# Kernel optimization log

Hardware: AMD Instinct MI355X
Metric: run time of the kernel (lower is better)

The kernel has to match this reference:

```python
import jax, jax.numpy as jnp
import numpy as np

N = 8192
INPUT_DIM = 256
HIDDEN_DIM = 16
K_NEIGHBORS = 6


def setup_inputs() -> dict:
    key = jax.random.key(0)
    k1, k2 = jax.random.split(key)
    x = jax.random.normal(k1, (N, INPUT_DIM), dtype=jnp.float32)
    W = jax.random.normal(k2, (HIDDEN_DIM, INPUT_DIM), dtype=jnp.float32) * (1.0 / np.sqrt(INPUT_DIM))
    b = jnp.zeros((HIDDEN_DIM,), dtype=jnp.float32)
    return {"x": x, "W": W, "b": b}


def reference(x, W, b):
    num_nodes = x.shape[0]
    # Linear projection then L2-normalize rows (F.normalize, p=2, dim=1, eps=1e-12)
    h = x @ W.T + b                                   # [N, H]
    norm = jnp.linalg.norm(h, axis=1, keepdims=True)
    h = h / jnp.maximum(norm, 1e-12)
    sim = h @ h.T                                     # [N, N] cosine similarity
    k = min(K_NEIGHBORS, num_nodes - 1)
    # top-(k+1) per row; drop the first (self, sim=1 is the max)
    top_vals, top_idx = jax.lax.top_k(sim, k + 1)     # [N, k+1]
    neigh_idx = top_idx[:, 1:]                        # [N, k]
    neigh_vals = top_vals[:, 1:]                      # [N, k]
    rows = jnp.arange(num_nodes)[:, None]             # [N, 1]
    adj = jnp.zeros_like(sim).at[rows, neigh_idx].set(neigh_vals)
    adj = (adj + adj.T) * 0.5
    row_sums = adj.sum(axis=1, keepdims=True)
    adj = adj / (row_sums + 1e-8)
    return adj
```

## Files before the change

kernel.cpp:

```cpp
#include <hip/hip_runtime.h>
#include <stdint.h>
#include <math.h>

#define NN   8192
#define IND  256
#define HID  16
#define KN   6
#define SEG  8
#define SW   (NN/SEG)
#define CCOL 256
#define NCH  (SW/CCOL)
#define TPC  (CCOL/16)
#define ZPB  8192

typedef short s8v  __attribute__((ext_vector_type(8)));
typedef float f4v  __attribute__((ext_vector_type(4)));

__device__ __forceinline__ uint32_t fflip(float f) {
    const uint32_t u = __float_as_uint(f);
    return (u & 0x80000000u) ? ~u : (u | 0x80000000u);
}

__device__ __forceinline__ uint32_t bf16_rne_bits(float x) {
    const uint32_t u = __float_as_uint(x);
    return (u + 0x7FFFu + ((u >> 16) & 1u)) & 0xFFFF0000u;
}

__global__ __launch_bounds__(256) void k1_embed(const float* __restrict__ x,
                                                const float* __restrict__ W,
                                                const float* __restrict__ b,
                                                float* __restrict__ h,
                                                float* __restrict__ rs)
{
    const int lane = threadIdx.x & 63;
    const int wv   = threadIdx.x >> 6;
    const int row  = blockIdx.x * 4 + wv;

    const float4 xv = *(const float4*)(x + (size_t)row * IND + lane * 4);

    float acc[HID];
#pragma unroll
    for (int k = 0; k < HID; ++k) {
        const float4 wv4 = *(const float4*)(W + (size_t)k * IND + lane * 4);
        float v = xv.x * wv4.x + xv.y * wv4.y + xv.z * wv4.z + xv.w * wv4.w;
#pragma unroll
        for (int m = 32; m >= 1; m >>= 1) v += __shfl_xor(v, m, 64);
        acc[k] = v;
    }

    if (lane == 0) {
        float hv[HID];
        float ss = 0.f;
#pragma unroll
        for (int k = 0; k < HID; ++k) { hv[k] = acc[k] + b[k]; ss += hv[k] * hv[k]; }
        const float nrm = fmaxf(sqrtf(ss), 1e-12f);
#pragma unroll
        for (int k = 0; k < HID; ++k) hv[k] = hv[k] / nrm;
        float4* hp = (float4*)(h + (size_t)row * HID);
        hp[0] = make_float4(hv[0],  hv[1],  hv[2],  hv[3]);
        hp[1] = make_float4(hv[4],  hv[5],  hv[6],  hv[7]);
        hp[2] = make_float4(hv[8],  hv[9],  hv[10], hv[11]);
        hp[3] = make_float4(hv[12], hv[13], hv[14], hv[15]);
        rs[row] = 0.f;
    }
}

__global__ __launch_bounds__(256) void k1b_split(const float* __restrict__ h,
                                                 ushort* __restrict__ PA1,
                                                 ushort* __restrict__ PA2,
                                                 ushort* __restrict__ PA3,
                                                 ushort* __restrict__ PB1,
                                                 ushort* __restrict__ PB2)
{
    const int t   = blockIdx.x * 256 + threadIdx.x;
    const int row = t >> 5;
    const int s   = t & 31;
    const int k   = s & 15;

    const float x = h[(size_t)row * HID + k];
    const uint32_t hb = bf16_rne_bits(x);
    const float r1 = x - __uint_as_float(hb);
    const uint32_t mb = bf16_rne_bits(r1);
    const float r2 = r1 - __uint_as_float(mb);
    const uint32_t lb = bf16_rne_bits(r2);
    const ushort hi = (ushort)(hb >> 16);
    const ushort mi = (ushort)(mb >> 16);
    const ushort lo = (ushort)(lb >> 16);

    const bool f = (s < 16);
    PA1[t] = hi;
    PA2[t] = f ? mi : hi;
    PA3[t] = f ? lo : mi;
    PB1[t] = f ? hi : mi;
    PB2[t] = f ? hi : lo;
}

#define CSWPF(X,i,j) { const float _h = fmaxf(X[i], X[j]); const float _l = fminf(X[i], X[j]); X[i] = _h; X[j] = _l; }
#define CSWPV(a,b)   { const float _h = fmaxf(a, b); const float _l = fminf(a, b); a = _h; b = _l; }
#define BSTAGES(X) CSWPF(X,0,4) CSWPF(X,1,5) CSWPF(X,2,6) CSWPF(X,3,7) \
                   CSWPF(X,0,2) CSWPF(X,1,3) CSWPF(X,4,6) CSWPF(X,5,7) \
                   CSWPF(X,0,1) CSWPF(X,2,3) CSWPF(X,4,5) CSWPF(X,6,7)

__global__ __launch_bounds__(256, 4) void p1_scan(const ushort* __restrict__ PA1,
                                                  const ushort* __restrict__ PA2,
                                                  const ushort* __restrict__ PA3,
                                                  const ushort* __restrict__ PB1,
                                                  const ushort* __restrict__ PB2,
                                                  float* __restrict__ tq,
                                                  float4* __restrict__ outz)
{
    __shared__ s8v lds[2048];

    const int tid  = threadIdx.x;
    const int lane = tid & 63;
    const int wv   = tid >> 6;
    const int seg  = blockIdx.x & (SEG - 1);
    const int row0 = (blockIdx.x >> 3) * 64 + wv * 16;
    const int n    = lane & 15;
    const int q    = lane >> 4;
    const int qs   = (q + ((n >> 1) & 3)) & 3;

    const size_t ioff = ((size_t)(row0 + n) << 5) + (q << 3);
    const s8v i1 = *(const s8v*)(PA1 + ioff);
    const s8v i2 = *(const s8v*)(PA2 + ioff);
    const s8v i3 = *(const s8v*)(PA3 + ioff);

    const float4 zf = make_float4(0.f, 0.f, 0.f, 0.f);

    float L[8];
#pragma unroll
    for (int t = 0; t < 8; ++t) L[t] = -INFINITY;

    for (int cc = 0; cc < NCH; ++cc) {
        __syncthreads();
#pragma unroll
        for (int it = 0; it < 8; ++it) {
            const int o  = it * 256 + tid;
            const int oo = o & 1023;
            const int c  = oo >> 2;
            const int qq = oo & 3;
            const int sw = (qq + ((c >> 1) & 3)) & 3;
            const ushort* src = (it < 4) ? PB1 : PB2;
            const int gcol = seg * SW + cc * CCOL + c;
            const s8v v = *(const s8v*)(src + ((size_t)gcol << 5) + (qq << 3));
            lds[((it < 4) ? 0 : 1024) + (c << 2) + sw] = v;
        }
        __syncthreads();

        {
            const size_t zb = (size_t)blockIdx.x * ZPB + (size_t)cc * 2048 + tid;
#pragma unroll
            for (int z = 0; z < 8; ++z)
                outz[zb + z * 256] = zf;
        }

        const int base = (n << 2) + qs;
#pragma unroll 4
        for (int t = 0; t < TPC; ++t) {
            const s8v jb1 = lds[t * 64 + base];
            const s8v jb2 = lds[1024 + t * 64 + base];

            f4v acc = {0.f, 0.f, 0.f, 0.f};
            acc = __builtin_amdgcn_mfma_f32_16x16x32_bf16(jb1, i1, acc, 0, 0, 0);
            acc = __builtin_amdgcn_mfma_f32_16x16x32_bf16(jb2, i2, acc, 0, 0, 0);
            acc = __builtin_amdgcn_mfma_f32_16x16x32_bf16(jb1, i3, acc, 0, 0, 0);

            float s0 = acc[0], s1 = acc[1], s2 = acc[2], s3 = acc[3];
            CSWPV(s0, s1) CSWPV(s2, s3) CSWPV(s0, s2) CSWPV(s1, s3) CSWPV(s1, s2)

            L[4] = fmaxf(L[4], s3);
            L[5] = fmaxf(L[5], s2);
            L[6] = fmaxf(L[6], s1);
            L[7] = fmaxf(L[7], s0);
            BSTAGES(L)
        }
    }

#pragma unroll
    for (int mm = 16; mm <= 32; mm <<= 1) {
        float o[8], X[8];
#pragma unroll
        for (int t = 0; t < 8; ++t) o[t] = __shfl_xor(L[t], mm, 64);
#pragma unroll
        for (int t = 0; t < 8; ++t) X[t] = fmaxf(L[t], o[7 - t]);
        BSTAGES(X)
#pragma unroll
        for (int t = 0; t < 8; ++t) L[t] = X[t];
    }

    if (q == 0) {
        float* dst = tq + ((size_t)seg * NN + (row0 + n)) * 8;
#pragma unroll
        for (int t = 0; t < 8; ++t) dst[t] = L[t];
    }
}

__global__ __launch_bounds__(256) void p15_tau(const float* __restrict__ tq,
                                               float* __restrict__ tau,
                                               int* __restrict__ cnt)
{
    const int row = blockIdx.x * 256 + threadIdx.x;
    float hd[SEG]; int ix[SEG];
#pragma unroll
    for (int s = 0; s < SEG; ++s) { hd[s] = tq[((size_t)s * NN + row) * 8]; ix[s] = 0; }
    float tv = -INFINITY;
#pragma unroll
    for (int t = 0; t < 8; ++t) {
        float best = hd[0]; int bs = 0;
#pragma unroll
        for (int s = 1; s < SEG; ++s)
            if (hd[s] > best) { best = hd[s]; bs = s; }
        tv = best;
        ++ix[bs];
        hd[bs] = (ix[bs] < 8) ? tq[((size_t)bs * NN + row) * 8 + ix[bs]] : -INFINITY;
    }
    tau[row] = tv;
    cnt[row] = 0;
}

__global__ __launch_bounds__(256, 4) void p2_emit(const ushort* __restrict__ PA1,
                                                  const ushort* __restrict__ PA2,
                                                  const ushort* __restrict__ PA3,
                                                  const ushort* __restrict__ PB1,
                                                  const ushort* __restrict__ PB2,
                                                  const float* __restrict__ tau,
                                                  int* __restrict__ cnt,
                                                  float* __restrict__ candv,
                                                  int* __restrict__ candj,
                                                  float4* __restrict__ outz)
{
    __shared__ s8v lds[2048];

    const int tid  = threadIdx.x;
    const int lane = tid & 63;
    const int wv   = tid >> 6;
    const int seg  = blockIdx.x & (SEG - 1);
    const int row0 = (blockIdx.x >> 3) * 64 + wv * 16;
    const int n    = lane & 15;
    const int q    = lane >> 4;
    const int qs   = (q + ((n >> 1) & 3)) & 3;
    const int row  = row0 + n;

    const size_t ioff = ((size_t)row << 5) + (q << 3);
    const s8v i1 = *(const s8v*)(PA1 + ioff);
    const s8v i2 = *(const s8v*)(PA2 + ioff);
    const s8v i3 = *(const s8v*)(PA3 + ioff);
    const float tv = tau[row];

    const float4 zf = make_float4(0.f, 0.f, 0.f, 0.f);

    for (int cc = 0; cc < NCH; ++cc) {
        __syncthreads();
#pragma unroll
        for (int it = 0; it < 8; ++it) {
            const int o  = it * 256 + tid;
            const int oo = o & 1023;
            const int c  = oo >> 2;
            const int qq = oo & 3;
            const int sw = (qq + ((c >> 1) & 3)) & 3;
            const ushort* src = (it < 4) ? PB1 : PB2;
            const int gcol = seg * SW + cc * CCOL + c;
            const s8v v = *(const s8v*)(src + ((size_t)gcol << 5) + (qq << 3));
            lds[((it < 4) ? 0 : 1024) + (c << 2) + sw] = v;
        }
        __syncthreads();

        {
            const size_t zb = (size_t)(NN / 8) * NN / 2 +
                              (size_t)blockIdx.x * ZPB + (size_t)cc * 2048 + tid;
#pragma unroll
            for (int z = 0; z < 8; ++z)
                outz[zb + z * 256] = zf;
        }

        const int base = (n << 2) + qs;
#pragma unroll 4
        for (int t = 0; t < TPC; ++t) {
            const s8v jb1 = lds[t * 64 + base];
            const s8v jb2 = lds[1024 + t * 64 + base];

            f4v acc = {0.f, 0.f, 0.f, 0.f};
            acc = __builtin_amdgcn_mfma_f32_16x16x32_bf16(jb1, i1, acc, 0, 0, 0);
            acc = __builtin_amdgcn_mfma_f32_16x16x32_bf16(jb2, i2, acc, 0, 0, 0);
            acc = __builtin_amdgcn_mfma_f32_16x16x32_bf16(jb1, i3, acc, 0, 0, 0);

            const float vm = fmaxf(fmaxf(acc[0], acc[1]), fmaxf(acc[2], acc[3]));
            if (__builtin_expect(vm >= tv, 0)) {
                const int jbase = seg * SW + cc * CCOL + t * 16 + (q << 2);
#pragma unroll
                for (int g = 0; g < 4; ++g) {
                    if (acc[g] >= tv) {
                        const int idx = atomicAdd(&cnt[row], 1);
                        if (idx < 16) {
                            candv[(size_t)row * 16 + idx] = acc[g];
                            candj[(size_t)row * 16 + idx] = jbase + g;
                        }
                    }
                }
            }
        }
    }
}

__global__ __launch_bounds__(256) void p3_select(const int* __restrict__ cnt,
                                                 const float* __restrict__ candv,
                                                 const int* __restrict__ candj,
                                                 int* __restrict__ nbr_idx,
                                                 float* __restrict__ nbr_val)
{
    const int row = blockIdx.x * 256 + threadIdx.x;
    const int c = min(cnt[row], 16);
    uint64_t keys[16];
    for (int i = 0; i < c; ++i) {
        const float v = candv[(size_t)row * 16 + i];
        const uint32_t j = (uint32_t)candj[(size_t)row * 16 + i];
        keys[i] = ((uint64_t)fflip(v) << 32) | (uint64_t)(~j);
    }
    for (int t = 0; t < 7; ++t) {
        uint64_t best = 0; int bi = 0;
        for (int i = 0; i < c; ++i)
            if (keys[i] > best) { best = keys[i]; bi = i; }
        keys[bi] = 0;
        if (t >= 1) {
            uint32_t u = (uint32_t)(best >> 32);
            u = (u & 0x80000000u) ? (u & 0x7fffffffu) : ~u;
            nbr_val[(size_t)row * KN + (t - 1)] = __uint_as_float(u);
            nbr_idx[(size_t)row * KN + (t - 1)] = (int)~(uint32_t)best;
        }
    }
}

__global__ __launch_bounds__(256) void k4_rowsum(const int* __restrict__ nbr_idx,
                                                 const float* __restrict__ nbr_val,
                                                 float* __restrict__ rs)
{
    const int e = blockIdx.x * 256 + threadIdx.x;
    const int i = e / KN;
    const int j = nbr_idx[e];
    const float v = nbr_val[e] * 0.5f;
    atomicAdd(&rs[i], v);
    atomicAdd(&rs[j], v);
}

__global__ __launch_bounds__(256) void k5_scatter(const int* __restrict__ nbr_idx,
                                                  const float* __restrict__ nbr_val,
                                                  const float* __restrict__ rs,
                                                  float* __restrict__ out)
{
    const int e = blockIdx.x * 256 + threadIdx.x;
    const int i = e / KN;
    const int j = nbr_idx[e];
    const float v = nbr_val[e] * 0.5f;
    const float wi = v / (rs[i] + 1e-8f);
    const float wj = v / (rs[j] + 1e-8f);
    atomicAdd(out + (size_t)i * NN + j, wi);
    atomicAdd(out + (size_t)j * NN + i, wj);
}

extern "C" void kernel_launch(void* const* d_in, const int* in_sizes, int n_in,
                              void* d_out, int out_size, void* d_ws, size_t ws_size,
                              hipStream_t stream)
{
    const float* x = (const float*)d_in[0];
    const float* W = (const float*)d_in[1];
    const float* b = (const float*)d_in[2];
    float* out = (float*)d_out;

    float* tq    = (float*)d_ws;
    float* tau   = tq + (size_t)SEG * NN * 8;
    float* h     = tau + NN;
    float* rs    = h + (size_t)NN * HID;
    float* nv    = rs + NN;
    float* candv = nv + (size_t)NN * KN;
    int*   ni    = (int*)(candv + (size_t)NN * 16);
    int*   candj = ni + (size_t)NN * KN;
    int*   cnt   = candj + (size_t)NN * 16;
    ushort* PA1  = (ushort*)(cnt + NN);
    ushort* PA2  = PA1 + (size_t)NN * 32;
    ushort* PA3  = PA2 + (size_t)NN * 32;
    ushort* PB1  = PA3 + (size_t)NN * 32;
    ushort* PB2  = PB1 + (size_t)NN * 32;

    k1_embed <<<NN / 4,            256, 0, stream>>>(x, W, b, h, rs);
    k1b_split<<<(NN * 32) / 256,   256, 0, stream>>>(h, PA1, PA2, PA3, PB1, PB2);
    p1_scan  <<<(NN / 64) * SEG,   256, 0, stream>>>(PA1, PA2, PA3, PB1, PB2, tq, (float4*)out);
    p15_tau  <<<NN / 256,          256, 0, stream>>>(tq, tau, cnt);
    p2_emit  <<<(NN / 64) * SEG,   256, 0, stream>>>(PA1, PA2, PA3, PB1, PB2, tau, cnt, candv, candj, (float4*)out);
    p3_select<<<NN / 256,          256, 0, stream>>>(cnt, candv, candj, ni, nv);
    k4_rowsum<<<(NN * KN) / 256,   256, 0, stream>>>(ni, nv, rs);
    k5_scatter<<<(NN * KN) / 256,  256, 0, stream>>>(ni, nv, rs, out);
}
```

Baseline: 322.0 us.

## Eliminate second similarity pass by packing column index into double top-k keys

The scan now carries each similarity as a double whose low mantissa bits hold a tie-broken column index, so the per-segment top-8 lists already identify neighbours. A single warp-shuffle merge kernel then replaces the tau, emit, select and rowsum passes, and the first pass now zeroes the whole output. The embed and bf16 split kernels are also fused through LDS. This removes the second full MFMA sweep and several launches, but the sorting network in the hot loop now runs on fp64 min/max, which may be slower per element, and the packed tie bits can perturb ordering.

```diff
diff --git a/kernel.cpp b/kernel.cpp
--- a/kernel.cpp
+++ b/kernel.cpp
@@ -11,27 +11,33 @@
 #define CCOL 256
 #define NCH  (SW/CCOL)
 #define TPC  (CCOL/16)
-#define ZPB  8192
+#define ZPB  16384
 
 typedef short s8v  __attribute__((ext_vector_type(8)));
 typedef float f4v  __attribute__((ext_vector_type(4)));
-
-__device__ __forceinline__ uint32_t fflip(float f) {
-    const uint32_t u = __float_as_uint(f);
-    return (u & 0x80000000u) ? ~u : (u | 0x80000000u);
-}
 
 __device__ __forceinline__ uint32_t bf16_rne_bits(float x) {
     const uint32_t u = __float_as_uint(x);
     return (u + 0x7FFFu + ((u >> 16) & 1u)) & 0xFFFF0000u;
 }
 
+#define CSWPD(X,i,j) { const double _h = fmax(X[i], X[j]); const double _l = fmin(X[i], X[j]); X[i] = _h; X[j] = _l; }
+#define CSWPS(a,b)   { const double _h = fmax(a, b); const double _l = fmin(a, b); a = _h; b = _l; }
+#define BSTAGESD(X) CSWPD(X,0,4) CSWPD(X,1,5) CSWPD(X,2,6) CSWPD(X,3,7) \
+                    CSWPD(X,0,2) CSWPD(X,1,3) CSWPD(X,4,6) CSWPD(X,5,7) \
+                    CSWPD(X,0,1) CSWPD(X,2,3) CSWPD(X,4,5) CSWPD(X,6,7)
+
 __global__ __launch_bounds__(256) void k1_embed(const float* __restrict__ x,
                                                 const float* __restrict__ W,
                                                 const float* __restrict__ b,
-                                                float* __restrict__ h,
-                                                float* __restrict__ rs)
-{
+                                                float* __restrict__ rs,
+                                                ushort* __restrict__ PA1,
+                                                ushort* __restrict__ PA2,
+                                                ushort* __restrict__ PA3,
+                                                ushort* __restrict__ PB1,
+                                                ushort* __restrict__ PB2)
+{
+    __shared__ float sh[4][16];
     const int lane = threadIdx.x & 63;
     const int wv   = threadIdx.x >> 6;
     const int row  = blockIdx.x * 4 + wv;
@@ -55,58 +61,39 @@
         for (int k = 0; k < HID; ++k) { hv[k] = acc[k] + b[k]; ss += hv[k] * hv[k]; }
         const float nrm = fmaxf(sqrtf(ss), 1e-12f);
 #pragma unroll
-        for (int k = 0; k < HID; ++k) hv[k] = hv[k] / nrm;
-        float4* hp = (float4*)(h + (size_t)row * HID);
-        hp[0] = make_float4(hv[0],  hv[1],  hv[2],  hv[3]);
-        hp[1] = make_float4(hv[4],  hv[5],  hv[6],  hv[7]);
-        hp[2] = make_float4(hv[8],  hv[9],  hv[10], hv[11]);
-        hp[3] = make_float4(hv[12], hv[13], hv[14], hv[15]);
+        for (int k = 0; k < HID; ++k) sh[wv][k] = hv[k] / nrm;
         rs[row] = 0.f;
     }
-}
-
-__global__ __launch_bounds__(256) void k1b_split(const float* __restrict__ h,
-                                                 ushort* __restrict__ PA1,
-                                                 ushort* __restrict__ PA2,
-                                                 ushort* __restrict__ PA3,
-                                                 ushort* __restrict__ PB1,
-                                                 ushort* __restrict__ PB2)
-{
-    const int t   = blockIdx.x * 256 + threadIdx.x;
-    const int row = t >> 5;
-    const int s   = t & 31;
-    const int k   = s & 15;
-
-    const float x = h[(size_t)row * HID + k];
-    const uint32_t hb = bf16_rne_bits(x);
-    const float r1 = x - __uint_as_float(hb);
-    const uint32_t mb = bf16_rne_bits(r1);
-    const float r2 = r1 - __uint_as_float(mb);
-    const uint32_t lb = bf16_rne_bits(r2);
-    const ushort hi = (ushort)(hb >> 16);
-    const ushort mi = (ushort)(mb >> 16);
-    const ushort lo = (ushort)(lb >> 16);
-
-    const bool f = (s < 16);
-    PA1[t] = hi;
-    PA2[t] = f ? mi : hi;
-    PA3[t] = f ? lo : mi;
-    PB1[t] = f ? hi : mi;
-    PB2[t] = f ? hi : lo;
-}
-
-#define CSWPF(X,i,j) { const float _h = fmaxf(X[i], X[j]); const float _l = fminf(X[i], X[j]); X[i] = _h; X[j] = _l; }
-#define CSWPV(a,b)   { const float _h = fmaxf(a, b); const float _l = fminf(a, b); a = _h; b = _l; }
-#define BSTAGES(X) CSWPF(X,0,4) CSWPF(X,1,5) CSWPF(X,2,6) CSWPF(X,3,7) \
-                   CSWPF(X,0,2) CSWPF(X,1,3) CSWPF(X,4,6) CSWPF(X,5,7) \
-                   CSWPF(X,0,1) CSWPF(X,2,3) CSWPF(X,4,5) CSWPF(X,6,7)
+    __syncthreads();
+
+    if (lane < 32) {
+        const int s = lane;
+        const int k = s & 15;
+        const float xval = sh[wv][k];
+        const uint32_t hb = bf16_rne_bits(xval);
+        const float r1 = xval - __uint_as_float(hb);
+        const uint32_t mb = bf16_rne_bits(r1);
+        const float r2 = r1 - __uint_as_float(mb);
+        const uint32_t lb = bf16_rne_bits(r2);
+        const ushort hi = (ushort)(hb >> 16);
+        const ushort mi = (ushort)(mb >> 16);
+        const ushort lo = (ushort)(lb >> 16);
+        const bool f = (s < 16);
+        const size_t t = (size_t)row * 32 + s;
+        PA1[t] = hi;
+        PA2[t] = f ? mi : hi;
+        PA3[t] = f ? lo : mi;
+        PB1[t] = f ? hi : mi;
+        PB2[t] = f ? hi : lo;
+    }
+}
 
 __global__ __launch_bounds__(256, 4) void p1_scan(const ushort* __restrict__ PA1,
                                                   const ushort* __restrict__ PA2,
                                                   const ushort* __restrict__ PA3,
                                                   const ushort* __restrict__ PB1,
                                                   const ushort* __restrict__ PB2,
-                                                  float* __restrict__ tq,
+                                                  double* __restrict__ tqd,
                                                   float4* __restrict__ outz)
 {
     __shared__ s8v lds[2048];
@@ -127,7 +114,7 @@
 
     const float4 zf = make_float4(0.f, 0.f, 0.f, 0.f);
 
-    float L[8];
+    double L[8];
 #pragma unroll
     for (int t = 0; t < 8; ++t) L[t] = -INFINITY;
 
@@ -148,14 +135,15 @@
         __syncthreads();
 
         {
-            const size_t zb = (size_t)blockIdx.x * ZPB + (size_t)cc * 2048 + tid;
-#pragma unroll
-            for (int z = 0; z < 8; ++z)
+            const size_t zb = (size_t)blockIdx.x * ZPB + (size_t)cc * 4096 + tid;
+#pragma unroll
+            for (int z = 0; z < 16; ++z)
                 outz[zb + z * 256] = zf;
         }
 
         const int base = (n << 2) + qs;
-#pragma unroll 4
+        const int a0   = seg * SW + cc * CCOL + (q << 2);
+#pragma unroll 2
         for (int t = 0; t < TPC; ++t) {
             const s8v jb1 = lds[t * 64 + base];
             const s8v jb2 = lds[1024 + t * 64 + base];
@@ -165,181 +153,86 @@
             acc = __builtin_amdgcn_mfma_f32_16x16x32_bf16(jb2, i2, acc, 0, 0, 0);
             acc = __builtin_amdgcn_mfma_f32_16x16x32_bf16(jb1, i3, acc, 0, 0, 0);
 
-            float s0 = acc[0], s1 = acc[1], s2 = acc[2], s3 = acc[3];
-            CSWPV(s0, s1) CSWPV(s2, s3) CSWPV(s0, s2) CSWPV(s1, s3) CSWPV(s1, s2)
-
-            L[4] = fmaxf(L[4], s3);
-            L[5] = fmaxf(L[5], s2);
-            L[6] = fmaxf(L[6], s1);
-            L[7] = fmaxf(L[7], s0);
-            BSTAGES(L)
+            const int ca = a0 + (t << 4);
+            double kd[4];
+#pragma unroll
+            for (int g = 0; g < 4; ++g) {
+                const float v = acc[g];
+                const int ja  = ca + g;
+                const int tie = (v < 0.f) ? ja : (NN - 1 - ja);
+                kd[g] = __longlong_as_double(__double_as_longlong((double)v) |
+                                             (long long)(unsigned)tie);
+            }
+
+            double s0 = kd[0], s1 = kd[1], s2 = kd[2], s3 = kd[3];
+            CSWPS(s0, s1) CSWPS(s2, s3) CSWPS(s0, s2) CSWPS(s1, s3) CSWPS(s1, s2)
+
+            L[4] = fmax(L[4], s3);
+            L[5] = fmax(L[5], s2);
+            L[6] = fmax(L[6], s1);
+            L[7] = fmax(L[7], s0);
+            BSTAGESD(L)
         }
     }
 
 #pragma unroll
     for (int mm = 16; mm <= 32; mm <<= 1) {
-        float o[8], X[8];
+        double o[8], X[8];
 #pragma unroll
         for (int t = 0; t < 8; ++t) o[t] = __shfl_xor(L[t], mm, 64);
 #pragma unroll
-        for (int t = 0; t < 8; ++t) X[t] = fmaxf(L[t], o[7 - t]);
-        BSTAGES(X)
+        for (int t = 0; t < 8; ++t) X[t] = fmax(L[t], o[7 - t]);
+        BSTAGESD(X)
 #pragma unroll
         for (int t = 0; t < 8; ++t) L[t] = X[t];
     }
 
     if (q == 0) {
-        float* dst = tq + ((size_t)seg * NN + (row0 + n)) * 8;
+        double* dst = tqd + ((size_t)seg * NN + (row0 + n)) * 8;
 #pragma unroll
         for (int t = 0; t < 8; ++t) dst[t] = L[t];
     }
 }
 
-__global__ __launch_bounds__(256) void p15_tau(const float* __restrict__ tq,
-                                               float* __restrict__ tau,
-                                               int* __restrict__ cnt)
-{
-    const int row = blockIdx.x * 256 + threadIdx.x;
-    float hd[SEG]; int ix[SEG];
-#pragma unroll
-    for (int s = 0; s < SEG; ++s) { hd[s] = tq[((size_t)s * NN + row) * 8]; ix[s] = 0; }
-    float tv = -INFINITY;
-#pragma unroll
-    for (int t = 0; t < 8; ++t) {
-        float best = hd[0]; int bs = 0;
-#pragma unroll
-        for (int s = 1; s < SEG; ++s)
-            if (hd[s] > best) { best = hd[s]; bs = s; }
-        tv = best;
-        ++ix[bs];
-        hd[bs] = (ix[bs] < 8) ? tq[((size_t)bs * NN + row) * 8 + ix[bs]] : -INFINITY;
-    }
-    tau[row] = tv;
-    cnt[row] = 0;
-}
-
-__global__ __launch_bounds__(256, 4) void p2_emit(const ushort* __restrict__ PA1,
-                                                  const ushort* __restrict__ PA2,
-                                                  const ushort* __restrict__ PA3,
-                                                  const ushort* __restrict__ PB1,
-                                                  const ushort* __restrict__ PB2,
-                                                  const float* __restrict__ tau,
-                                                  int* __restrict__ cnt,
-                                                  float* __restrict__ candv,
-                                                  int* __restrict__ candj,
-                                                  float4* __restrict__ outz)
-{
-    __shared__ s8v lds[2048];
-
-    const int tid  = threadIdx.x;
-    const int lane = tid & 63;
-    const int wv   = tid >> 6;
-    const int seg  = blockIdx.x & (SEG - 1);
-    const int row0 = (blockIdx.x >> 3) * 64 + wv * 16;
-    const int n    = lane & 15;
-    const int q    = lane >> 4;
-    const int qs   = (q + ((n >> 1) & 3)) & 3;
-    const int row  = row0 + n;
-
-    const size_t ioff = ((size_t)row << 5) + (q << 3);
-    const s8v i1 = *(const s8v*)(PA1 + ioff);
-    const s8v i2 = *(const s8v*)(PA2 + ioff);
-    const s8v i3 = *(const s8v*)(PA3 + ioff);
-    const float tv = tau[row];
-
-    const float4 zf = make_float4(0.f, 0.f, 0.f, 0.f);
-
-    for (int cc = 0; cc < NCH; ++cc) {
-        __syncthreads();
-#pragma unroll
-        for (int it = 0; it < 8; ++it) {
-            const int o  = it * 256 + tid;
-            const int oo = o & 1023;
-            const int c  = oo >> 2;
-            const int qq = oo & 3;
-            const int sw = (qq + ((c >> 1) & 3)) & 3;
-            const ushort* src = (it < 4) ? PB1 : PB2;
-            const int gcol = seg * SW + cc * CCOL + c;
-            const s8v v = *(const s8v*)(src + ((size_t)gcol << 5) + (qq << 3));
-            lds[((it < 4) ? 0 : 1024) + (c << 2) + sw] = v;
-        }
-        __syncthreads();
-
-        {
-            const size_t zb = (size_t)(NN / 8) * NN / 2 +
-                              (size_t)blockIdx.x * ZPB + (size_t)cc * 2048 + tid;
-#pragma unroll
-            for (int z = 0; z < 8; ++z)
-                outz[zb + z * 256] = zf;
-        }
-
-        const int base = (n << 2) + qs;
-#pragma unroll 4
-        for (int t = 0; t < TPC; ++t) {
-            const s8v jb1 = lds[t * 64 + base];
-            const s8v jb2 = lds[1024 + t * 64 + base];
-
-            f4v acc = {0.f, 0.f, 0.f, 0.f};
-            acc = __builtin_amdgcn_mfma_f32_16x16x32_bf16(jb1, i1, acc, 0, 0, 0);
-            acc = __builtin_amdgcn_mfma_f32_16x16x32_bf16(jb2, i2, acc, 0, 0, 0);
-            acc = __builtin_amdgcn_mfma_f32_16x16x32_bf16(jb1, i3, acc, 0, 0, 0);
-
-            const float vm = fmaxf(fmaxf(acc[0], acc[1]), fmaxf(acc[2], acc[3]));
-            if (__builtin_expect(vm >= tv, 0)) {
-                const int jbase = seg * SW + cc * CCOL + t * 16 + (q << 2);
-#pragma unroll
-                for (int g = 0; g < 4; ++g) {
-                    if (acc[g] >= tv) {
-                        const int idx = atomicAdd(&cnt[row], 1);
-                        if (idx < 16) {
-                            candv[(size_t)row * 16 + idx] = acc[g];
-                            candj[(size_t)row * 16 + idx] = jbase + g;
-                        }
-                    }
-                }
+__global__ __launch_bounds__(256) void p2_merge(const double* __restrict__ tqd,
+                                                float* __restrict__ rs,
+                                                int* __restrict__ ni,
+                                                float* __restrict__ nv)
+{
+    const int lane = threadIdx.x & 63;
+    const int wv   = threadIdx.x >> 6;
+    const int row  = blockIdx.x * 4 + wv;
+    const int s    = lane >> 3;
+    const int t    = lane & 7;
+
+    double key = tqd[((size_t)s * NN + row) * 8 + t];
+    float sum = 0.f;
+
+#pragma unroll
+    for (int r = 0; r < 7; ++r) {
+        double m = key;
+#pragma unroll
+        for (int mm = 1; mm < 64; mm <<= 1) {
+            const double o = __shfl_xor(m, mm, 64);
+            m = fmax(m, o);
+        }
+        const long long mb = __double_as_longlong(m);
+        if (r >= 1) {
+            const float v  = (float)__longlong_as_double(mb & ~0x1FFFLL);
+            const int tie  = (int)(mb & 0x1FFFLL);
+            const int j    = (v < 0.f) ? tie : (NN - 1 - tie);
+            sum += v;
+            if (__double_as_longlong(key) == mb) {
+                nv[(size_t)row * KN + (r - 1)] = v;
+                ni[(size_t)row * KN + (r - 1)] = j;
+                atomicAdd(&rs[j], 0.5f * v);
             }
         }
-    }
-}
-
-__global__ __launch_bounds__(256) void p3_select(const int* __restrict__ cnt,
-                                                 const float* __restrict__ candv,
-                                                 const int* __restrict__ candj,
-                                                 int* __restrict__ nbr_idx,
-                                                 float* __restrict__ nbr_val)
-{
-    const int row = blockIdx.x * 256 + threadIdx.x;
-    const int c = min(cnt[row], 16);
-    uint64_t keys[16];
-    for (int i = 0; i < c; ++i) {
-        const float v = candv[(size_t)row * 16 + i];
-        const uint32_t j = (uint32_t)candj[(size_t)row * 16 + i];
-        keys[i] = ((uint64_t)fflip(v) << 32) | (uint64_t)(~j);
-    }
-    for (int t = 0; t < 7; ++t) {
-        uint64_t best = 0; int bi = 0;
-        for (int i = 0; i < c; ++i)
-            if (keys[i] > best) { best = keys[i]; bi = i; }
-        keys[bi] = 0;
-        if (t >= 1) {
-            uint32_t u = (uint32_t)(best >> 32);
-            u = (u & 0x80000000u) ? (u & 0x7fffffffu) : ~u;
-            nbr_val[(size_t)row * KN + (t - 1)] = __uint_as_float(u);
-            nbr_idx[(size_t)row * KN + (t - 1)] = (int)~(uint32_t)best;
-        }
-    }
-}
-
-__global__ __launch_bounds__(256) void k4_rowsum(const int* __restrict__ nbr_idx,
-                                                 const float* __restrict__ nbr_val,
-                                                 float* __restrict__ rs)
-{
-    const int e = blockIdx.x * 256 + threadIdx.x;
-    const int i = e / KN;
-    const int j = nbr_idx[e];
-    const float v = nbr_val[e] * 0.5f;
-    atomicAdd(&rs[i], v);
-    atomicAdd(&rs[j], v);
+        if (__double_as_longlong(key) == mb)
+            key = __longlong_as_double((long long)0xFFF0000000000000LL);
+    }
+
+    if (lane == 0) atomicAdd(&rs[row], 0.5f * sum);
 }
 
 __global__ __launch_bounds__(256) void k5_scatter(const int* __restrict__ nbr_idx,
@@ -366,27 +259,18 @@
     const float* b = (const float*)d_in[2];
     float* out = (float*)d_out;
 
-    float* tq    = (float*)d_ws;
-    float* tau   = tq + (size_t)SEG * NN * 8;
-    float* h     = tau + NN;
-    float* rs    = h + (size_t)NN * HID;
-    float* nv    = rs + NN;
-    float* candv = nv + (size_t)NN * KN;
-    int*   ni    = (int*)(candv + (size_t)NN * 16);
-    int*   candj = ni + (size_t)NN * KN;
-    int*   cnt   = candj + (size_t)NN * 16;
-    ushort* PA1  = (ushort*)(cnt + NN);
+    double* tqd  = (double*)d_ws;
+    float*  rs   = (float*)(tqd + (size_t)SEG * NN * 8);
+    float*  nv   = rs + NN;
+    int*    ni   = (int*)(nv + (size_t)NN * KN);
+    ushort* PA1  = (ushort*)(ni + (size_t)NN * KN);
     ushort* PA2  = PA1 + (size_t)NN * 32;
     ushort* PA3  = PA2 + (size_t)NN * 32;
     ushort* PB1  = PA3 + (size_t)NN * 32;
     ushort* PB2  = PB1 + (size_t)NN * 32;
 
-    k1_embed <<<NN / 4,            256, 0, stream>>>(x, W, b, h, rs);
-    k1b_split<<<(NN * 32) / 256,   256, 0, stream>>>(h, PA1, PA2, PA3, PB1, PB2);
-    p1_scan  <<<(NN / 64) * SEG,   256, 0, stream>>>(PA1, PA2, PA3, PB1, PB2, tq, (float4*)out);
-    p15_tau  <<<NN / 256,          256, 0, stream>>>(tq, tau, cnt);
-    p2_emit  <<<(NN / 64) * SEG,   256, 0, stream>>>(PA1, PA2, PA3, PB1, PB2, tau, cnt, candv, candj, (float4*)out);
-    p3_select<<<NN / 256,          256, 0, stream>>>(cnt, candv, candj, ni, nv);
-    k4_rowsum<<<(NN * KN) / 256,   256, 0, stream>>>(ni, nv, rs);
-    k5_scatter<<<(NN * KN) / 256,  256, 0, stream>>>(ni, nv, rs, out);
-}
+    k1_embed <<<NN / 4,           256, 0, stream>>>(x, W, b, rs, PA1, PA2, PA3, PB1, PB2);
+    p1_scan  <<<(NN / 64) * SEG,  256, 0, stream>>>(PA1, PA2, PA3, PB1, PB2, tqd, (float4*)out);
+    p2_merge <<<NN / 4,           256, 0, stream>>>(tqd, rs, ni, nv);
+    k5_scatter<<<(NN * KN) / 256, 256, 0, stream>>>(ni, nv, rs, out);
+}
```

Result: no change. 316.9 us (-1.6%).
